# Kernel optimization log

Measured on AMD Instinct MI355X. Metric: run time of the kernel, lower is better.

## Reference

```python
import jax, jax.numpy as jnp
import numpy as np

N_USERS = 50000
N_ENTITIES = 250000
N_RELATIONS = 24
EMBED_DIM = 128
RELATION_DIM = 128
KG_BATCH = 16384
KG_L2_LAMBDA = 1e-5


def _l2_loss_mean(x):
    # mean over batch of (||x||^2 / 2)
    return jnp.mean(jnp.sum(x * x, axis=1) / 2.0)


def setup_inputs() -> dict:
    key = jax.random.key(0)
    k1, k2, k3, k4, k5, k6, k7 = jax.random.split(key, 7)
    n_total = N_ENTITIES + N_USERS
    # xavier-uniform-like init scale
    s_e = float(np.sqrt(6.0 / (n_total + EMBED_DIM)))
    s_r = float(np.sqrt(6.0 / (N_RELATIONS + RELATION_DIM)))
    s_m = float(np.sqrt(6.0 / (EMBED_DIM + RELATION_DIM)))
    entity_user_embed = jax.random.uniform(k1, (n_total, EMBED_DIM), jnp.float32, -s_e, s_e)
    relation_embed = jax.random.uniform(k2, (N_RELATIONS, RELATION_DIM), jnp.float32, -s_r, s_r)
    trans_M = jax.random.uniform(k3, (N_RELATIONS, EMBED_DIM, RELATION_DIM), jnp.float32, -s_m, s_m)
    h = jax.random.randint(k4, (KG_BATCH,), 0, n_total, dtype=jnp.int64 if jax.config.jax_enable_x64 else jnp.int32)
    r = jax.random.randint(k5, (KG_BATCH,), 0, N_RELATIONS, dtype=h.dtype)
    pos_t = jax.random.randint(k6, (KG_BATCH,), 0, n_total, dtype=h.dtype)
    neg_t = jax.random.randint(k7, (KG_BATCH,), 0, n_total, dtype=h.dtype)
    return {
        "entity_user_embed": entity_user_embed,
        "relation_embed": relation_embed,
        "trans_M": trans_M,
        "h": h,
        "r": r,
        "pos_t": pos_t,
        "neg_t": neg_t,
    }


def reference(entity_user_embed, relation_embed, trans_M, h, r, pos_t, neg_t):
    # KGAT.calc_kg_loss (mode='train_kg')
    r_embed = relation_embed[r]            # [B, R]
    W_r = trans_M[r]                       # [B, E, R] per-edge TransR matrix (gather)
    h_embed = entity_user_embed[h]         # [B, E]
    pos_t_embed = entity_user_embed[pos_t] # [B, E]
    neg_t_embed = entity_user_embed[neg_t] # [B, E]

    # bmm([B,1,E], [B,E,R]) -> [B,R]
    r_mul_h = jnp.einsum('be,ber->br', h_embed, W_r)
    r_mul_pos_t = jnp.einsum('be,ber->br', pos_t_embed, W_r)
    r_mul_neg_t = jnp.einsum('be,ber->br', neg_t_embed, W_r)

    pos_score = jnp.sum(jnp.square(r_mul_h + r_embed - r_mul_pos_t), axis=1)
    neg_score = jnp.sum(jnp.square(r_mul_h + r_embed - r_mul_neg_t), axis=1)

    kg_loss = jnp.mean(-jax.nn.log_sigmoid(neg_score - pos_score))
    l2_loss = (_l2_loss_mean(r_mul_h) + _l2_loss_mean(r_embed)
               + _l2_loss_mean(r_mul_pos_t) + _l2_loss_mean(r_mul_neg_t))
    return kg_loss + KG_L2_LAMBDA * l2_loss
```

## Files before the change

### kernel.cpp

```cpp
#include <hip/hip_runtime.h>
#include <math.h>

#define KG_B    16384
#define KG_D    128
#define KG_NR   24
#define KG_TM   32
#define KG_BPAD (KG_B + KG_NR * KG_TM)
#define KG_NGRP (KG_BPAD / KG_TM)

#define WS_BSUM KG_BPAD
#define WS_PREW_BYTES 131072

typedef __attribute__((ext_vector_type(8))) short bf16x8;
typedef __attribute__((ext_vector_type(4))) float f32x4;

__device__ __forceinline__ unsigned bf16r(float f) {
    return (__float_as_uint(f) + 0x8000u) >> 16;
}
__device__ __forceinline__ unsigned pack2(float lo, float hi) {
    return bf16r(lo) | (bf16r(hi) << 16);
}

__global__ __launch_bounds__(1024) void kg_sort_prep(const int* __restrict__ r,
                                                     const float* __restrict__ M,
                                                     int* __restrict__ perm,
                                                     unsigned short* __restrict__ preW) {
    __shared__ int cntw[16][25];
    __shared__ int basew[16][25];
    __shared__ int pbase_s[24];
    __shared__ int cnt_tot[24];
    __shared__ int total_s;
    __shared__ __align__(16) unsigned short sWp[KG_D * KG_D];

    const int t = threadIdx.x;

    if (blockIdx.x != 0) {
        const int k  = blockIdx.x - 1;
        const int e  = t >> 3;
        const int c0 = (t & 7) * 16;
        const float* src = M + ((size_t)k << 14) + (size_t)e * KG_D + c0;
        float4 rw[4];
#pragma unroll
        for (int f = 0; f < 4; ++f) rw[f] = ((const float4*)src)[f];
#pragma unroll
        for (int dc = 0; dc < 16; ++dc) {
            const int col = c0 + dc;
            const float v = ((const float*)&rw[0])[dc];
            sWp[col * KG_D + e] = (unsigned short)bf16r(v);
        }
        __syncthreads();
        uint4* dst = (uint4*)(preW + ((size_t)k << 14));
        const uint4* s4 = (const uint4*)sWp;
        dst[2 * t]     = s4[2 * t];
        dst[2 * t + 1] = s4[2 * t + 1];
        return;
    }

    const int w = t >> 6;
    int* cz = &cntw[0][0];
    for (int i = t; i < 16 * 25; i += 1024) cz[i] = 0;
    __syncthreads();

    int kt[16];
#pragma unroll
    for (int j = 0; j < 16; ++j) kt[j] = r[j * 1024 + t];
#pragma unroll
    for (int j = 0; j < 16; ++j) atomicAdd(&cntw[w][kt[j]], 1);
    __syncthreads();

    if (t < 24) {
        int s = 0;
        for (int w2 = 0; w2 < 16; ++w2) { basew[w2][t] = s; s += cntw[w2][t]; }
        cnt_tot[t] = s;
    }
    __syncthreads();
    if (t == 0) {
        int run = 0;
        for (int k = 0; k < 24; ++k) {
            pbase_s[k] = run;
            run += (cnt_tot[k] + (KG_TM - 1)) & ~(KG_TM - 1);
        }
        total_s = run;
    }
    __syncthreads();
    if (t < 24)
        for (int w2 = 0; w2 < 16; ++w2) basew[w2][t] += pbase_s[t];
    for (int i = t; i < 16 * 25; i += 1024) cz[i] = 0;
    __syncthreads();

#pragma unroll
    for (int j = 0; j < 16; ++j) {
        const int k = kt[j];
        const int pos = basew[w][k] + atomicAdd(&cntw[w][k], 1);
        perm[pos] = j * 1024 + t;
    }
    __syncthreads();

    if (t < 24) {
        const int e0 = pbase_s[t] + cnt_tot[t];
        const int e1 = pbase_s[t] + ((cnt_tot[t] + (KG_TM - 1)) & ~(KG_TM - 1));
        for (int p = e0; p < e1; ++p) perm[p] = -1;
    }
    for (int i = total_s + t; i < KG_BPAD; i += 1024) perm[i] = -1;
}

__global__ __launch_bounds__(256, 4) void kg_main(
    const float* __restrict__ ent, const float* __restrict__ rel,
    const unsigned short* __restrict__ preW,
    const int* __restrict__ h,     const int* __restrict__ r,
    const int* __restrict__ pt,    const int* __restrict__ nt,
    const int* __restrict__ perm,  float* __restrict__ bsum)
{
    __shared__ __align__(16) unsigned short sX[3 * KG_TM * KG_D];
    __shared__ float sScr[2][KG_TM][4];

    const int tid   = threadIdx.x;
    const int slot0 = blockIdx.x * KG_TM;
    const int p0    = perm[slot0];
    if (p0 < 0) {
        if (tid == 0) bsum[blockIdx.x] = 0.f;
        return;
    }
    const int rb = __builtin_amdgcn_readfirstlane(r[p0]);

    {
        const int g  = tid >> 3;
        const int e0 = (tid & 7) * 16;
        const int pg = perm[slot0 + g];
        const int bb = pg < 0 ? p0 : pg;
        const int idx3[3] = { h[bb], pt[bb], nt[bb] };
        const int sw = (g & 7) << 3;
#pragma unroll
        for (int t3 = 0; t3 < 3; ++t3) {
            const float* src = ent + (size_t)idx3[t3] * KG_D + e0;
            const float4 f0 = ((const float4*)src)[0];
            const float4 f1 = ((const float4*)src)[1];
            const float4 f2 = ((const float4*)src)[2];
            const float4 f3 = ((const float4*)src)[3];
            uint4 u0, u1;
            u0.x = pack2(f0.x, f0.y); u0.y = pack2(f0.z, f0.w);
            u0.z = pack2(f1.x, f1.y); u0.w = pack2(f1.z, f1.w);
            u1.x = pack2(f2.x, f2.y); u1.y = pack2(f2.z, f2.w);
            u1.z = pack2(f3.x, f3.y); u1.w = pack2(f3.z, f3.w);
            unsigned short* base = sX + t3 * (KG_TM * KG_D) + g * KG_D;
            *(uint4*)(base + ((e0    ) ^ sw)) = u0;
            *(uint4*)(base + ((e0 + 8) ^ sw)) = u1;
        }
    }
    __syncthreads();

    const int l   = tid & 63;
    const int w   = tid >> 6;
    const int rt  = w & 1;
    const int chs = w >> 1;
    const int li  = l & 15;
    const int kq  = l >> 4;

    const int ar  = rt * 16 + li;
    const int asw = (ar & 7) << 3;

    const unsigned short* __restrict__ preWk = preW + ((size_t)rb << 14);

    f32x4 acc[3][4];
#pragma unroll
    for (int t3 = 0; t3 < 3; ++t3)
#pragma unroll
        for (int n = 0; n < 4; ++n) acc[t3][n] = (f32x4)0.f;

#pragma unroll
    for (int kk = 0; kk < 4; ++kk) {
        const int e0 = kk * 32 + kq * 8;
        bf16x8 af[3];
#pragma unroll
        for (int t3 = 0; t3 < 3; ++t3)
            af[t3] = *(const bf16x8*)&sX[t3 * (KG_TM * KG_D) + ar * KG_D + (e0 ^ asw)];
#pragma unroll
        for (int n = 0; n < 4; ++n) {
            const int col = chs * 64 + n * 16 + li;
            const bf16x8 bfr = *(const bf16x8*)&preWk[col * KG_D + e0];
            acc[0][n] = __builtin_amdgcn_mfma_f32_16x16x32_bf16(af[0], bfr, acc[0][n], 0, 0, 0);
            acc[1][n] = __builtin_amdgcn_mfma_f32_16x16x32_bf16(af[1], bfr, acc[1][n], 0, 0, 0);
            acc[2][n] = __builtin_amdgcn_mfma_f32_16x16x32_bf16(af[2], bfr, acc[2][n], 0, 0, 0);
        }
    }

    float ps[4] = {0,0,0,0}, ns[4] = {0,0,0,0}, sq[4] = {0,0,0,0};
    const float* relrow = rel + (size_t)rb * KG_D + chs * 64;
#pragma unroll
    for (int n = 0; n < 4; ++n) {
        const float rv = relrow[n * 16 + li];
#pragma unroll
        for (int j = 0; j < 4; ++j) {
            const float va = acc[0][n][j];
            const float vp = acc[1][n][j];
            const float vn = acc[2][n][j];
            const float s  = va + rv;
            const float dp = s - vp;
            const float dn = s - vn;
            ps[j] += dp * dp;
            ns[j] += dn * dn;
            sq[j] += va * va + vp * vp + vn * vn + rv * rv;
        }
    }
#pragma unroll
    for (int j = 0; j < 4; ++j)
#pragma unroll
        for (int m = 1; m < 16; m <<= 1) {
            ps[j] += __shfl_xor(ps[j], m);
            ns[j] += __shfl_xor(ns[j], m);
            sq[j] += __shfl_xor(sq[j], m);
        }

    if (li == 0) {
#pragma unroll
        for (int j = 0; j < 4; ++j) {
            const int row = rt * 16 + kq * 4 + j;
            sScr[chs][row][0] = ps[j];
            sScr[chs][row][1] = ns[j];
            sScr[chs][row][2] = sq[j];
        }
    }
    __syncthreads();

    if (tid < 64) {
        float term = 0.f;
        if (tid < KG_TM) {
            const int row = tid;
            const float P = sScr[0][row][0] + sScr[1][row][0];
            const float N = sScr[0][row][1] + sScr[1][row][1];
            const float S = sScr[0][row][2] + sScr[1][row][2];
            const int pg = perm[slot0 + row];
            if (pg >= 0) {
                const float x = P - N;
                term = fmaxf(x, 0.f) + log1pf(expf(-fabsf(x)))
                     + 5e-6f * S;
            }
        }
#pragma unroll
        for (int off = 16; off > 0; off >>= 1) term += __shfl_down(term, off);
        if (tid == 0) bsum[blockIdx.x] = term;
    }
}

__global__ __launch_bounds__(256) void kg_final(const float* __restrict__ bsum,
                                                float* __restrict__ out) {
    __shared__ float s[256];
    const int t = threadIdx.x;
    float acc = 0.f;
    for (int i = t; i < KG_NGRP; i += 256) acc += bsum[i];
    s[t] = acc;
    __syncthreads();
    for (int off = 128; off > 0; off >>= 1) {
        if (t < off) s[t] += s[t + off];
        __syncthreads();
    }
    if (t == 0) out[0] = s[0] * (1.0f / (float)KG_B);
}

extern "C" void kernel_launch(void* const* d_in, const int* in_sizes, int n_in,
                              void* d_out, int out_size, void* d_ws, size_t ws_size,
                              hipStream_t stream) {
    const float* ent = (const float*)d_in[0];
    const float* rel = (const float*)d_in[1];
    const float* M   = (const float*)d_in[2];
    const int*   h   = (const int*)d_in[3];
    const int*   r   = (const int*)d_in[4];
    const int*   pt  = (const int*)d_in[5];
    const int*   nt  = (const int*)d_in[6];

    int*            perm = (int*)d_ws;
    float*          bsum = (float*)d_ws + WS_BSUM;
    unsigned short* preW = (unsigned short*)((char*)d_ws + WS_PREW_BYTES);
    float*          out  = (float*)d_out;

    kg_sort_prep<<<1 + KG_NR, 1024, 0, stream>>>(r, M, perm, preW);
    kg_main     <<<KG_NGRP, 256, 0, stream>>>(ent, rel, preW, h, r, pt, nt, perm, bsum);
    kg_final    <<<1, 256, 0, stream>>>(bsum, out);
}
```

Measured before the change: 28.62 us.

## Pre-gather entity rows to bf16 in prep kernel and DMA into LDS

The prep kernel gains 192 extra blocks that gather the h/pos/neg entity rows, convert them to bf16 and write them in batch order into a workspace buffer, overlapping with the sort and W-transpose work. The main kernel then pulls its 32-row tiles straight into LDS with global_load_lds in a fragment-friendly layout, so it no longer does scattered fp32 loads and conversion itself. The cost is an extra write and read of about 12 MB of bf16 data through global memory. The path is used only when the workspace is large enough, with a fallback to the old code.

```diff
diff --git a/kernel.cpp b/kernel.cpp
--- a/kernel.cpp
+++ b/kernel.cpp
@@ -8,8 +8,10 @@
 #define KG_BPAD (KG_B + KG_NR * KG_TM)
 #define KG_NGRP (KG_BPAD / KG_TM)
 
-#define WS_BSUM KG_BPAD
 #define WS_PREW_BYTES 131072
+#define WS_XP_BYTES   1048576
+#define WS_XP_SIZE    (3 * KG_B * KG_D * 2)
+#define WS_NEED_XP    ((size_t)WS_XP_BYTES + (size_t)WS_XP_SIZE)
 
 typedef __attribute__((ext_vector_type(8))) short bf16x8;
 typedef __attribute__((ext_vector_type(4))) float f32x4;
@@ -21,10 +23,14 @@
     return bf16r(lo) | (bf16r(hi) << 16);
 }
 
-__global__ __launch_bounds__(1024) void kg_sort_prep(const int* __restrict__ r,
-                                                     const float* __restrict__ M,
-                                                     int* __restrict__ perm,
-                                                     unsigned short* __restrict__ preW) {
+template<int XP>
+__global__ __launch_bounds__(1024) void kg_sort_prep(
+    const int* __restrict__ r,   const float* __restrict__ M,
+    const int* __restrict__ h,   const int* __restrict__ pt,
+    const int* __restrict__ nt,  const float* __restrict__ ent,
+    int* __restrict__ perm,      unsigned short* __restrict__ preW,
+    unsigned short* __restrict__ Xp)
+{
     __shared__ int cntw[16][25];
     __shared__ int basew[16][25];
     __shared__ int pbase_s[24];
@@ -34,6 +40,31 @@
 
     const int t = threadIdx.x;
 
+    if (XP && blockIdx.x > KG_NR) {
+        const int pb = blockIdx.x - 1 - KG_NR;
+        const int qr = pb * 1024 + t;
+        const int t3 = qr >> 16;
+        const int b  = (qr >> 2) & (KG_B - 1);
+        const int qu = qr & 3;
+        const int* idxarr = (t3 == 0) ? h : ((t3 == 1) ? pt : nt);
+        const int idx = idxarr[b];
+        const float* src = ent + (size_t)idx * KG_D + qu * 32;
+        float4 f[8];
+#pragma unroll
+        for (int i = 0; i < 8; ++i) f[i] = ((const float4*)src)[i];
+        unsigned u[16];
+#pragma unroll
+        for (int i = 0; i < 8; ++i) {
+            u[2 * i]     = pack2(f[i].x, f[i].y);
+            u[2 * i + 1] = pack2(f[i].z, f[i].w);
+        }
+        uint4* dst = (uint4*)(Xp + ((size_t)t3 * KG_B + b) * KG_D + qu * 32);
+#pragma unroll
+        for (int i = 0; i < 4; ++i)
+            dst[i] = make_uint4(u[4 * i], u[4 * i + 1], u[4 * i + 2], u[4 * i + 3]);
+        return;
+    }
+
     if (blockIdx.x != 0) {
         const int k  = blockIdx.x - 1;
         const int e  = t >> 3;
@@ -104,9 +135,11 @@
     for (int i = total_s + t; i < KG_BPAD; i += 1024) perm[i] = -1;
 }
 
+template<int XP>
 __global__ __launch_bounds__(256, 4) void kg_main(
     const float* __restrict__ ent, const float* __restrict__ rel,
     const unsigned short* __restrict__ preW,
+    const unsigned short* __restrict__ Xp,
     const int* __restrict__ h,     const int* __restrict__ r,
     const int* __restrict__ pt,    const int* __restrict__ nt,
     const int* __restrict__ perm,  float* __restrict__ bsum)
@@ -123,7 +156,25 @@
     }
     const int rb = __builtin_amdgcn_readfirstlane(r[p0]);
 
-    {
+    const int l  = tid & 63;
+    const int wv = tid >> 6;
+
+    if (XP) {
+        const int pv = perm[slot0 + (l & 31)];
+        const int bb = pv < 0 ? p0 : pv;
+        const int half = l >> 5;
+#pragma unroll
+        for (int q = 0; q < 6; ++q) {
+            const int i = wv * 6 + q;
+            const int s = 2 * i + half;
+            const int o = s & 15, t3 = s >> 4;
+            const char* src = (const char*)Xp
+                + (((size_t)t3 * KG_B + (size_t)bb) << 8) + (o << 4);
+            __builtin_amdgcn_global_load_lds(
+                (const unsigned int*)src,
+                (unsigned int*)((char*)sX + i * 1024), 16, 0, 0);
+        }
+    } else {
         const int g  = tid >> 3;
         const int e0 = (tid & 7) * 16;
         const int pg = perm[slot0 + g];
@@ -149,10 +200,8 @@
     }
     __syncthreads();
 
-    const int l   = tid & 63;
-    const int w   = tid >> 6;
-    const int rt  = w & 1;
-    const int chs = w >> 1;
+    const int rt  = wv & 1;
+    const int chs = wv >> 1;
     const int li  = l & 15;
     const int kq  = l >> 4;
 
@@ -161,26 +210,33 @@
 
     const unsigned short* __restrict__ preWk = preW + ((size_t)rb << 14);
 
-    f32x4 acc[3][4];
+    f32x4 accf[3][4];
 #pragma unroll
     for (int t3 = 0; t3 < 3; ++t3)
 #pragma unroll
-        for (int n = 0; n < 4; ++n) acc[t3][n] = (f32x4)0.f;
+        for (int n = 0; n < 4; ++n) accf[t3][n] = (f32x4)0.f;
 
 #pragma unroll
     for (int kk = 0; kk < 4; ++kk) {
+        bf16x8 af[3];
+        if (XP) {
+#pragma unroll
+            for (int t3 = 0; t3 < 3; ++t3)
+                af[t3] = *(const bf16x8*)&sX[(t3 * 16 + kk * 4 + kq) * 256 + ar * 8];
+        } else {
+            const int e0 = kk * 32 + kq * 8;
+#pragma unroll
+            for (int t3 = 0; t3 < 3; ++t3)
+                af[t3] = *(const bf16x8*)&sX[t3 * (KG_TM * KG_D) + ar * KG_D + (e0 ^ asw)];
+        }
         const int e0 = kk * 32 + kq * 8;
-        bf16x8 af[3];
-#pragma unroll
-        for (int t3 = 0; t3 < 3; ++t3)
-            af[t3] = *(const bf16x8*)&sX[t3 * (KG_TM * KG_D) + ar * KG_D + (e0 ^ asw)];
 #pragma unroll
         for (int n = 0; n < 4; ++n) {
             const int col = chs * 64 + n * 16 + li;
             const bf16x8 bfr = *(const bf16x8*)&preWk[col * KG_D + e0];
-            acc[0][n] = __builtin_amdgcn_mfma_f32_16x16x32_bf16(af[0], bfr, acc[0][n], 0, 0, 0);
-            acc[1][n] = __builtin_amdgcn_mfma_f32_16x16x32_bf16(af[1], bfr, acc[1][n], 0, 0, 0);
-            acc[2][n] = __builtin_amdgcn_mfma_f32_16x16x32_bf16(af[2], bfr, acc[2][n], 0, 0, 0);
+            accf[0][n] = __builtin_amdgcn_mfma_f32_16x16x32_bf16(af[0], bfr, accf[0][n], 0, 0, 0);
+            accf[1][n] = __builtin_amdgcn_mfma_f32_16x16x32_bf16(af[1], bfr, accf[1][n], 0, 0, 0);
+            accf[2][n] = __builtin_amdgcn_mfma_f32_16x16x32_bf16(af[2], bfr, accf[2][n], 0, 0, 0);
         }
     }
 
@@ -191,9 +247,9 @@
         const float rv = relrow[n * 16 + li];
 #pragma unroll
         for (int j = 0; j < 4; ++j) {
-            const float va = acc[0][n][j];
-            const float vp = acc[1][n][j];
-            const float vn = acc[2][n][j];
+            const float va = accf[0][n][j];
+            const float vp = accf[1][n][j];
+            const float vn = accf[2][n][j];
             const float s  = va + rv;
             const float dp = s - vp;
             const float dn = s - vn;
@@ -269,11 +325,21 @@
     const int*   nt  = (const int*)d_in[6];
 
     int*            perm = (int*)d_ws;
-    float*          bsum = (float*)d_ws + WS_BSUM;
+    float*          bsum = (float*)d_ws + KG_BPAD;
     unsigned short* preW = (unsigned short*)((char*)d_ws + WS_PREW_BYTES);
+    unsigned short* Xp   = (unsigned short*)((char*)d_ws + WS_XP_BYTES);
     float*          out  = (float*)d_out;
 
-    kg_sort_prep<<<1 + KG_NR, 1024, 0, stream>>>(r, M, perm, preW);
-    kg_main     <<<KG_NGRP, 256, 0, stream>>>(ent, rel, preW, h, r, pt, nt, perm, bsum);
-    kg_final    <<<1, 256, 0, stream>>>(bsum, out);
-}
+    if (ws_size >= WS_NEED_XP) {
+        kg_sort_prep<1><<<1 + KG_NR + 192, 1024, 0, stream>>>(r, M, h, pt, nt, ent,
+                                                              perm, preW, Xp);
+        kg_main<1>   <<<KG_NGRP, 256, 0, stream>>>(ent, rel, preW, Xp,
+                                                   h, r, pt, nt, perm, bsum);
+    } else {
+        kg_sort_prep<0><<<1 + KG_NR, 1024, 0, stream>>>(r, M, h, pt, nt, ent,
+                                                        perm, preW, Xp);
+        kg_main<0>   <<<KG_NGRP, 256, 0, stream>>>(ent, rel, preW, Xp,
+                                                   h, r, pt, nt, perm, bsum);
+    }
+    kg_final<<<1, 256, 0, stream>>>(bsum, out);
+}
```

New measurement: 30.93 us. +8.1%, slower.
